# Kernel tuning notes

Hardware: AMD Instinct MI355X
Metric: run time of the kernel (lower is better)

The kernel has to match this reference:

```python
import jax, jax.numpy as jnp
import numpy as np

N_NODES = 100000
N_EDGES = 1600000
D_IN = 64
D_HID = 64
N_LAYERS = 3


def setup_inputs() -> dict:
    key = jax.random.key(0)
    ks = jax.random.split(key, 10)
    inp = {
        "node_feat": jax.random.normal(ks[0], (N_NODES, D_IN), dtype=jnp.float32),
        "src": jax.random.randint(ks[1], (N_EDGES,), 0, N_NODES, dtype=jnp.int32),
        "dst": jax.random.randint(ks[2], (N_EDGES,), 0, N_NODES, dtype=jnp.int32),
        "graph_len": jnp.ones((1,), dtype=jnp.int32) * N_NODES,
    }
    # GraphConv weights: shape (in_feats, out_feats), applied as feat @ W + b (DGL xavier-style init)
    dims = [D_IN] + [D_HID] * N_LAYERS
    for i in range(N_LAYERS):
        scale = float(np.sqrt(2.0 / (dims[i] + dims[i + 1])))
        inp[f"W{i}"] = jax.random.normal(ks[3 + i], (dims[i], dims[i + 1]), dtype=jnp.float32) * scale
        inp[f"b{i}"] = jnp.zeros((dims[i + 1],), dtype=jnp.float32)
    return inp


def reference(node_feat, src, dst, graph_len, W0, b0, W1, b1, W2, b2):
    n = node_feat.shape[0]
    e = src.shape[0]
    ones = jnp.ones((e,), dtype=node_feat.dtype)
    # DGL GraphConv norm='both': src-side out-degree^{-1/2}, dst-side in-degree^{-1/2}, clamp(min=1)
    deg_out = jax.ops.segment_sum(ones, src, num_segments=n)
    deg_in = jax.ops.segment_sum(ones, dst, num_segments=n)
    inv_sqrt_out = jax.lax.rsqrt(jnp.clip(deg_out, 1.0, None))[:, None]  # [N,1]
    inv_sqrt_in = jax.lax.rsqrt(jnp.clip(deg_in, 1.0, None))[:, None]    # [N,1]

    def graph_conv(x, W, b):
        msg = (x * inv_sqrt_out)[src]                              # [E,F] gather
        agg = jax.ops.segment_sum(msg, dst, num_segments=n)        # [N,F] scatter-add
        return (agg * inv_sqrt_in) @ W + b                         # SpMM result -> dense linear

    xs = []
    h = node_feat
    for W, b in ((W0, b0), (W1, b1), (W2, b2)):
        h = jax.nn.relu(graph_conv(h, W, b))
        xs.append(h)

    # Faithful to source: torch.sum(x, dim=1) -> per-node scalar [N]; concat over layers -> [3N]
    x_pool = jnp.concatenate([x.sum(axis=1) for x in xs], axis=-1)
    xs_cat = jnp.concatenate(xs, axis=-1)  # [N, 3*H]
    return x_pool, xs_cat
```

## Files before the change

kernel.cpp:

```cpp
#include <hip/hip_runtime.h>


#define TPB 256
#define CAPB 16384
#define CAP_S2 10240

__device__ __forceinline__ unsigned short f2bf(float f) {
  unsigned u = __float_as_uint(f);
  u += 0x7fff + ((u >> 16) & 1);
  return (unsigned short)(u >> 16);
}
__device__ __forceinline__ float bflo(unsigned u) { return __uint_as_float(u << 16); }
__device__ __forceinline__ float bfhi(unsigned u) { return __uint_as_float(u & 0xffff0000u); }

__global__ void init_cursors(int* __restrict__ cur_s, int* __restrict__ cur_d) {
  int t = threadIdx.x;
  cur_s[t] = t * CAPB;
  cur_d[t] = t * CAPB;
}

__global__ __launch_bounds__(256) void scatter_both(
    const int* __restrict__ src, const int* __restrict__ dst, int e,
    int* __restrict__ cur_s, int* __restrict__ cur_d,
    int* __restrict__ srcbuf, unsigned* __restrict__ edges1) {
  __shared__ int hs[256], hd[256];
  int t = threadIdx.x, b = blockIdx.x;
  hs[t] = 0; hd[t] = 0;
  __syncthreads();
  int base = b * 4096;
  int sv[16], dv[16];
  #pragma unroll
  for (int k = 0; k < 4; k++) {
    int i = base + 4 * t + 1024 * k;
    if (i + 3 < e) {
      int4 s4 = *(const int4*)&src[i];
      int4 d4 = *(const int4*)&dst[i];
      sv[4*k] = s4.x; sv[4*k+1] = s4.y; sv[4*k+2] = s4.z; sv[4*k+3] = s4.w;
      dv[4*k] = d4.x; dv[4*k+1] = d4.y; dv[4*k+2] = d4.z; dv[4*k+3] = d4.w;
    } else {
      #pragma unroll
      for (int j = 0; j < 4; j++) {
        int idx = i + j;
        if (idx < e) { sv[4*k+j] = src[idx]; dv[4*k+j] = dst[idx]; }
        else { sv[4*k+j] = -1; dv[4*k+j] = -1; }
      }
    }
  }
  #pragma unroll
  for (int k = 0; k < 16; k++) {
    if (dv[k] >= 0) {
      atomicAdd(&hs[sv[k] >> 9], 1);
      atomicAdd(&hd[dv[k] >> 9], 1);
    }
  }
  __syncthreads();
  int bs = hs[t], bd = hd[t];
  hs[t] = bs ? atomicAdd(&cur_s[t], bs) : 0;
  hd[t] = bd ? atomicAdd(&cur_d[t], bd) : 0;
  __syncthreads();
  #pragma unroll
  for (int k = 0; k < 16; k++) {
    if (dv[k] >= 0) {
      int ps = atomicAdd(&hs[sv[k] >> 9], 1);
      srcbuf[ps] = sv[k];
      int pd = atomicAdd(&hd[dv[k] >> 9], 1);
      edges1[pd] = ((unsigned)sv[k] << 9) | (unsigned)(dv[k] & 511);
    }
  }
}

__global__ __launch_bounds__(256) void sort_deg_cast(
    const unsigned* __restrict__ edges1, const int* __restrict__ srcbuf,
    const int* __restrict__ cur_s, const int* __restrict__ cur_d,
    const float* __restrict__ node_feat,
    int* __restrict__ row_beg, int* __restrict__ row_end,
    float* __restrict__ inv_in, float* __restrict__ inv_out,
    unsigned short* __restrict__ xb, int* __restrict__ col, int n) {
  __shared__ int sOut[CAP_S2];
  __shared__ int hist[512], cur[512];
  __shared__ int psum[256];
  __shared__ int dhist[512];
  __shared__ float sInv[512];
  int b = blockIdx.x, t = threadIdx.x;
  int sbase = b * CAPB;
  int es = cur_s[b];
  int ed = cur_d[b];
  int rstart = b << 9;
  int nrows = min(512, n - rstart);
  hist[t] = 0; hist[t + 256] = 0;
  dhist[t] = 0; dhist[t + 256] = 0;
  __syncthreads();
  for (int i = sbase + t; i < ed; i += TPB) atomicAdd(&hist[edges1[i] & 511u], 1);
  for (int i = sbase + t; i < es; i += TPB) atomicAdd(&dhist[srcbuf[i] & 511], 1);
  __syncthreads();
  #pragma unroll
  for (int k = 0; k < 2; k++) {
    int r = t + k * 256;
    if (r < nrows) {
      float iv = rsqrtf(fmaxf((float)dhist[r], 1.0f));
      sInv[r] = iv;
      inv_out[rstart + r] = iv;
    }
  }
  int h0 = hist[2 * t], h1 = hist[2 * t + 1];
  psum[t] = h0 + h1; __syncthreads();
  for (int off = 1; off < 256; off <<= 1) {
    int a = (t >= off) ? psum[t - off] : 0;
    __syncthreads(); psum[t] += a; __syncthreads();
  }
  int ex = psum[t] - (h0 + h1);
  cur[2 * t] = ex; cur[2 * t + 1] = ex + h0;
  if (2 * t < nrows) {
    row_beg[rstart + 2 * t] = sbase + ex;
    row_end[rstart + 2 * t] = sbase + ex + h0;
    inv_in[rstart + 2 * t] = rsqrtf(fmaxf((float)h0, 1.0f));
  }
  if (2 * t + 1 < nrows) {
    row_beg[rstart + 2 * t + 1] = sbase + ex + h0;
    row_end[rstart + 2 * t + 1] = sbase + ex + h0 + h1;
    inv_in[rstart + 2 * t + 1] = rsqrtf(fmaxf((float)h1, 1.0f));
  }
  __syncthreads();
  for (int i = sbase + t; i < ed; i += TPB) {
    unsigned v = edges1[i];
    int pos = atomicAdd(&cur[v & 511u], 1);
    int svv = (int)(v >> 9);
    if (pos < CAP_S2) sOut[pos] = svv;
    else col[sbase + pos] = svv;
  }
  __syncthreads();
  int m = min(ed - sbase, CAP_S2);
  for (int k = t; k < m; k += TPB) col[sbase + k] = sOut[k];
  int total4 = nrows * 16;
  const float* xbase = node_feat + (size_t)rstart * 64;
  unsigned short* obase = xb + (size_t)rstart * 64;
  for (int u = t; u < total4; u += TPB) {
    int r = u >> 4;
    float sc = sInv[r];
    float4 v = *(const float4*)&xbase[(size_t)u * 4];
    ushort4 o;
    o.x = f2bf(v.x * sc); o.y = f2bf(v.y * sc);
    o.z = f2bf(v.z * sc); o.w = f2bf(v.w * sc);
    *(ushort4*)&obase[(size_t)u * 4] = o;
  }
}

__global__ __launch_bounds__(256) void spmm_bf16(
    const unsigned short* __restrict__ xb,
    const int* __restrict__ row_beg, const int* __restrict__ row_end,
    const int* __restrict__ col,
    float* __restrict__ agg, int n) {
  int wid = (blockIdx.x * TPB + threadIdx.x) >> 6;
  if (wid >= n) return;
  int lane = threadIdx.x & 63;
  int g = lane >> 3;
  int l8 = (lane & 7) << 3;
  int s = row_beg[wid], e = row_end[wid];
  float a0 = 0, a1 = 0, a2 = 0, a3 = 0, a4 = 0, a5 = 0, a6 = 0, a7 = 0;
  for (int i = s + g; i < e; i += 32) {
    int ec = e - 1;
    int i1 = i + 8, i2 = i + 16, i3 = i + 24;
    int c0 = col[i];
    int c1 = col[min(i1, ec)];
    int c2 = col[min(i2, ec)];
    int c3 = col[min(i3, ec)];
    float m1 = (i1 < e) ? 1.f : 0.f;
    float m2 = (i2 < e) ? 1.f : 0.f;
    float m3 = (i3 < e) ? 1.f : 0.f;
    uint4 r0 = *(const uint4*)&xb[(size_t)c0 * 64 + l8];
    uint4 r1 = *(const uint4*)&xb[(size_t)c1 * 64 + l8];
    uint4 r2 = *(const uint4*)&xb[(size_t)c2 * 64 + l8];
    uint4 r3 = *(const uint4*)&xb[(size_t)c3 * 64 + l8];
    a0 += bflo(r0.x); a1 += bfhi(r0.x); a2 += bflo(r0.y); a3 += bfhi(r0.y);
    a4 += bflo(r0.z); a5 += bfhi(r0.z); a6 += bflo(r0.w); a7 += bfhi(r0.w);
    a0 = fmaf(m1, bflo(r1.x), a0); a1 = fmaf(m1, bfhi(r1.x), a1);
    a2 = fmaf(m1, bflo(r1.y), a2); a3 = fmaf(m1, bfhi(r1.y), a3);
    a4 = fmaf(m1, bflo(r1.z), a4); a5 = fmaf(m1, bfhi(r1.z), a5);
    a6 = fmaf(m1, bflo(r1.w), a6); a7 = fmaf(m1, bfhi(r1.w), a7);
    a0 = fmaf(m2, bflo(r2.x), a0); a1 = fmaf(m2, bfhi(r2.x), a1);
    a2 = fmaf(m2, bflo(r2.y), a2); a3 = fmaf(m2, bfhi(r2.y), a3);
    a4 = fmaf(m2, bflo(r2.z), a4); a5 = fmaf(m2, bfhi(r2.z), a5);
    a6 = fmaf(m2, bflo(r2.w), a6); a7 = fmaf(m2, bfhi(r2.w), a7);
    a0 = fmaf(m3, bflo(r3.x), a0); a1 = fmaf(m3, bfhi(r3.x), a1);
    a2 = fmaf(m3, bflo(r3.y), a2); a3 = fmaf(m3, bfhi(r3.y), a3);
    a4 = fmaf(m3, bflo(r3.z), a4); a5 = fmaf(m3, bfhi(r3.z), a5);
    a6 = fmaf(m3, bflo(r3.w), a6); a7 = fmaf(m3, bfhi(r3.w), a7);
  }
  a0 += __shfl_xor(a0, 8); a0 += __shfl_xor(a0, 16); a0 += __shfl_xor(a0, 32);
  a1 += __shfl_xor(a1, 8); a1 += __shfl_xor(a1, 16); a1 += __shfl_xor(a1, 32);
  a2 += __shfl_xor(a2, 8); a2 += __shfl_xor(a2, 16); a2 += __shfl_xor(a2, 32);
  a3 += __shfl_xor(a3, 8); a3 += __shfl_xor(a3, 16); a3 += __shfl_xor(a3, 32);
  a4 += __shfl_xor(a4, 8); a4 += __shfl_xor(a4, 16); a4 += __shfl_xor(a4, 32);
  a5 += __shfl_xor(a5, 8); a5 += __shfl_xor(a5, 16); a5 += __shfl_xor(a5, 32);
  a6 += __shfl_xor(a6, 8); a6 += __shfl_xor(a6, 16); a6 += __shfl_xor(a6, 32);
  a7 += __shfl_xor(a7, 8); a7 += __shfl_xor(a7, 16); a7 += __shfl_xor(a7, 32);
  if (g == 0) {
    float4 lo = {a0, a1, a2, a3};
    float4 hi = {a4, a5, a6, a7};
    *(float4*)&agg[(size_t)wid * 64 + l8] = lo;
    *(float4*)&agg[(size_t)wid * 64 + l8 + 4] = hi;
  }
}

__global__ __launch_bounds__(256) void gemm_relu_pool(
    const float* __restrict__ agg, const float* __restrict__ inv_in,
    const float* __restrict__ inv_out,
    const float* __restrict__ W, const float* __restrict__ bias,
    float* __restrict__ out_cat, float* __restrict__ out_pool,
    unsigned short* __restrict__ xb_next, int n) {
  __shared__ float sW[64 * 64];
  __shared__ float sXT[64][68];
  int t = threadIdx.x;
  int row0 = blockIdx.x * 64;
  for (int i4 = t * 4; i4 < 4096; i4 += 1024)
    *(float4*)&sW[i4] = *(const float4*)&W[i4];
  for (int i = t; i < 4096; i += TPB) {
    int r = i >> 6, f = i & 63;
    int row = row0 + r;
    sXT[f][r] = (row < n) ? agg[(size_t)row * 64 + f] * inv_in[row] : 0.f;
  }
  __syncthreads();
  int tj = t & 15, tr = t >> 4;
  int j4 = tj << 2, r4 = tr << 2;
  const float4 bv = *(const float4*)&bias[j4];
  float4 a0 = bv, a1 = bv, a2 = bv, a3 = bv;
  #pragma unroll 8
  for (int f = 0; f < 64; f++) {
    float4 w  = *(const float4*)&sW[f * 64 + j4];
    float4 xv = *(const float4*)&sXT[f][r4];
    a0.x = fmaf(xv.x, w.x, a0.x); a0.y = fmaf(xv.x, w.y, a0.y);
    a0.z = fmaf(xv.x, w.z, a0.z); a0.w = fmaf(xv.x, w.w, a0.w);
    a1.x = fmaf(xv.y, w.x, a1.x); a1.y = fmaf(xv.y, w.y, a1.y);
    a1.z = fmaf(xv.y, w.z, a1.z); a1.w = fmaf(xv.y, w.w, a1.w);
    a2.x = fmaf(xv.z, w.x, a2.x); a2.y = fmaf(xv.z, w.y, a2.y);
    a2.z = fmaf(xv.z, w.z, a2.z); a2.w = fmaf(xv.z, w.w, a2.w);
    a3.x = fmaf(xv.w, w.x, a3.x); a3.y = fmaf(xv.w, w.y, a3.y);
    a3.z = fmaf(xv.w, w.z, a3.z); a3.w = fmaf(xv.w, w.w, a3.w);
  }
  float4 accs[4] = {a0, a1, a2, a3};
  #pragma unroll
  for (int ri = 0; ri < 4; ri++) {
    int row = row0 + r4 + ri;
    if (row < n) {
      float4 h = accs[ri];
      h.x = fmaxf(h.x, 0.f); h.y = fmaxf(h.y, 0.f);
      h.z = fmaxf(h.z, 0.f); h.w = fmaxf(h.w, 0.f);
      *(float4*)&out_cat[(size_t)row * 192 + j4] = h;
      if (xb_next) {
        float sc = inv_out[row];
        ushort4 o;
        o.x = f2bf(h.x * sc); o.y = f2bf(h.y * sc);
        o.z = f2bf(h.z * sc); o.w = f2bf(h.w * sc);
        *(ushort4*)&xb_next[(size_t)row * 64 + j4] = o;
      }
      float part = h.x + h.y + h.z + h.w;
      part += __shfl_xor(part, 1);
      part += __shfl_xor(part, 2);
      part += __shfl_xor(part, 4);
      part += __shfl_xor(part, 8);
      if (tj == 0) out_pool[row] = part;
    }
  }
}


extern "C" void kernel_launch(void* const* d_in, const int* in_sizes, int n_in,
                              void* d_out, int out_size, void* d_ws, size_t ws_size,
                              hipStream_t stream) {
  const float* node_feat = (const float*)d_in[0];
  const int* src = (const int*)d_in[1];
  const int* dst = (const int*)d_in[2];
  const float* Ws[3] = {(const float*)d_in[4], (const float*)d_in[6], (const float*)d_in[8]};
  const float* bs[3] = {(const float*)d_in[5], (const float*)d_in[7], (const float*)d_in[9]};
  float* out = (float*)d_out;
  int n = in_sizes[0] / 64;
  int e = in_sizes[1];
  int nbb = (n + 511) >> 9;
  int nblk = (e + 4095) / 4096;
  size_t slots = (size_t)nbb * CAPB;

  char* p = (char*)d_ws;
  float* agg = (float*)p;       p += (size_t)n * 64 * sizeof(float);
  unsigned short* xb = (unsigned short*)p; p += (size_t)n * 64 * sizeof(unsigned short);
  float* inv_out = (float*)p;   p += (size_t)n * sizeof(float);
  float* inv_in = (float*)p;    p += (size_t)n * sizeof(float);
  int* row_beg = (int*)p;       p += (size_t)n * sizeof(int);
  int* row_end = (int*)p;       p += (size_t)n * sizeof(int);
  int* cur_s = (int*)p;         p += 256 * sizeof(int);
  int* cur_d = (int*)p;         p += 256 * sizeof(int);
  unsigned* edges1 = (unsigned*)p; p += slots * sizeof(unsigned);
  int* srcbuf = (int*)p;        p += slots * sizeof(int);
  int* col = (int*)p;           p += slots * sizeof(int);

  init_cursors<<<1, 256, 0, stream>>>(cur_s, cur_d);
  scatter_both<<<nblk, TPB, 0, stream>>>(src, dst, e, cur_s, cur_d, srcbuf, edges1);
  sort_deg_cast<<<nbb, TPB, 0, stream>>>(edges1, srcbuf, cur_s, cur_d, node_feat,
                                         row_beg, row_end, inv_in, inv_out, xb, col, n);

  float* cat_base = out + (size_t)3 * n;
  for (int layer = 0; layer < 3; layer++) {
    spmm_bf16<<<(n + 3) / 4, TPB, 0, stream>>>(xb, row_beg, row_end, col, agg, n);
    gemm_relu_pool<<<(n + 63) / 64, TPB, 0, stream>>>(agg, inv_in, inv_out, Ws[layer], bs[layer],
        cat_base + (size_t)layer * 64, out + (size_t)layer * n,
        (layer < 2) ? xb : (unsigned short*)nullptr, n);
  }
}
```

Baseline: 357.0 us.

## Fuse SpMM aggregation into the GEMM/ReLU/pool kernel with ping-pong bf16 buffers

The separate SpMM kernel and GEMM kernel are merged into one 512-thread kernel. Each wave aggregates 16 destination rows and writes the scaled sums straight into the shared-memory transposed tile, so the 128-row GEMM runs on it without the fp32 agg buffer ever going to global memory. Two bf16 feature buffers alternate between layers, because a layer now reads the previous features while it writes the next ones. This removes the agg global write and re-read and halves the number of launches. In exchange each wave processes its rows one after another before the block barrier, so fewer independent gathers are in flight and some latency hiding is lost.

```diff
diff --git a/kernel.cpp b/kernel.cpp
--- a/kernel.cpp
+++ b/kernel.cpp
@@ -145,79 +145,77 @@
   }
 }
 
-__global__ __launch_bounds__(256) void spmm_bf16(
+__global__ __launch_bounds__(512) void spmm_gemm(
     const unsigned short* __restrict__ xb,
     const int* __restrict__ row_beg, const int* __restrict__ row_end,
     const int* __restrict__ col,
-    float* __restrict__ agg, int n) {
-  int wid = (blockIdx.x * TPB + threadIdx.x) >> 6;
-  if (wid >= n) return;
-  int lane = threadIdx.x & 63;
-  int g = lane >> 3;
-  int l8 = (lane & 7) << 3;
-  int s = row_beg[wid], e = row_end[wid];
-  float a0 = 0, a1 = 0, a2 = 0, a3 = 0, a4 = 0, a5 = 0, a6 = 0, a7 = 0;
-  for (int i = s + g; i < e; i += 32) {
-    int ec = e - 1;
-    int i1 = i + 8, i2 = i + 16, i3 = i + 24;
-    int c0 = col[i];
-    int c1 = col[min(i1, ec)];
-    int c2 = col[min(i2, ec)];
-    int c3 = col[min(i3, ec)];
-    float m1 = (i1 < e) ? 1.f : 0.f;
-    float m2 = (i2 < e) ? 1.f : 0.f;
-    float m3 = (i3 < e) ? 1.f : 0.f;
-    uint4 r0 = *(const uint4*)&xb[(size_t)c0 * 64 + l8];
-    uint4 r1 = *(const uint4*)&xb[(size_t)c1 * 64 + l8];
-    uint4 r2 = *(const uint4*)&xb[(size_t)c2 * 64 + l8];
-    uint4 r3 = *(const uint4*)&xb[(size_t)c3 * 64 + l8];
-    a0 += bflo(r0.x); a1 += bfhi(r0.x); a2 += bflo(r0.y); a3 += bfhi(r0.y);
-    a4 += bflo(r0.z); a5 += bfhi(r0.z); a6 += bflo(r0.w); a7 += bfhi(r0.w);
-    a0 = fmaf(m1, bflo(r1.x), a0); a1 = fmaf(m1, bfhi(r1.x), a1);
-    a2 = fmaf(m1, bflo(r1.y), a2); a3 = fmaf(m1, bfhi(r1.y), a3);
-    a4 = fmaf(m1, bflo(r1.z), a4); a5 = fmaf(m1, bfhi(r1.z), a5);
-    a6 = fmaf(m1, bflo(r1.w), a6); a7 = fmaf(m1, bfhi(r1.w), a7);
-    a0 = fmaf(m2, bflo(r2.x), a0); a1 = fmaf(m2, bfhi(r2.x), a1);
-    a2 = fmaf(m2, bflo(r2.y), a2); a3 = fmaf(m2, bfhi(r2.y), a3);
-    a4 = fmaf(m2, bflo(r2.z), a4); a5 = fmaf(m2, bfhi(r2.z), a5);
-    a6 = fmaf(m2, bflo(r2.w), a6); a7 = fmaf(m2, bfhi(r2.w), a7);
-    a0 = fmaf(m3, bflo(r3.x), a0); a1 = fmaf(m3, bfhi(r3.x), a1);
-    a2 = fmaf(m3, bflo(r3.y), a2); a3 = fmaf(m3, bfhi(r3.y), a3);
-    a4 = fmaf(m3, bflo(r3.z), a4); a5 = fmaf(m3, bfhi(r3.z), a5);
-    a6 = fmaf(m3, bflo(r3.w), a6); a7 = fmaf(m3, bfhi(r3.w), a7);
-  }
-  a0 += __shfl_xor(a0, 8); a0 += __shfl_xor(a0, 16); a0 += __shfl_xor(a0, 32);
-  a1 += __shfl_xor(a1, 8); a1 += __shfl_xor(a1, 16); a1 += __shfl_xor(a1, 32);
-  a2 += __shfl_xor(a2, 8); a2 += __shfl_xor(a2, 16); a2 += __shfl_xor(a2, 32);
-  a3 += __shfl_xor(a3, 8); a3 += __shfl_xor(a3, 16); a3 += __shfl_xor(a3, 32);
-  a4 += __shfl_xor(a4, 8); a4 += __shfl_xor(a4, 16); a4 += __shfl_xor(a4, 32);
-  a5 += __shfl_xor(a5, 8); a5 += __shfl_xor(a5, 16); a5 += __shfl_xor(a5, 32);
-  a6 += __shfl_xor(a6, 8); a6 += __shfl_xor(a6, 16); a6 += __shfl_xor(a6, 32);
-  a7 += __shfl_xor(a7, 8); a7 += __shfl_xor(a7, 16); a7 += __shfl_xor(a7, 32);
-  if (g == 0) {
-    float4 lo = {a0, a1, a2, a3};
-    float4 hi = {a4, a5, a6, a7};
-    *(float4*)&agg[(size_t)wid * 64 + l8] = lo;
-    *(float4*)&agg[(size_t)wid * 64 + l8 + 4] = hi;
-  }
-}
-
-__global__ __launch_bounds__(256) void gemm_relu_pool(
-    const float* __restrict__ agg, const float* __restrict__ inv_in,
-    const float* __restrict__ inv_out,
+    const float* __restrict__ inv_in, const float* __restrict__ inv_out,
     const float* __restrict__ W, const float* __restrict__ bias,
     float* __restrict__ out_cat, float* __restrict__ out_pool,
     unsigned short* __restrict__ xb_next, int n) {
   __shared__ float sW[64 * 64];
-  __shared__ float sXT[64][68];
+  __shared__ float sXT[64][132];
   int t = threadIdx.x;
-  int row0 = blockIdx.x * 64;
-  for (int i4 = t * 4; i4 < 4096; i4 += 1024)
+  int row0 = blockIdx.x << 7;
+  for (int i4 = t * 4; i4 < 4096; i4 += 2048)
     *(float4*)&sW[i4] = *(const float4*)&W[i4];
-  for (int i = t; i < 4096; i += TPB) {
-    int r = i >> 6, f = i & 63;
-    int row = row0 + r;
-    sXT[f][r] = (row < n) ? agg[(size_t)row * 64 + f] * inv_in[row] : 0.f;
+  int lane = t & 63;
+  int g = lane >> 3;
+  int l8 = (lane & 7) << 3;
+  int wv = t >> 6;
+  for (int k = 0; k < 16; k++) {
+    int rl = wv * 16 + k;
+    int row = row0 + rl;
+    float v = 0.f;
+    if (row < n) {
+      float a0 = 0, a1 = 0, a2 = 0, a3 = 0, a4 = 0, a5 = 0, a6 = 0, a7 = 0;
+      int s = row_beg[row], e = row_end[row];
+      for (int i = s + g; i < e; i += 32) {
+        int ec = e - 1;
+        int i1 = i + 8, i2 = i + 16, i3 = i + 24;
+        int c0 = col[i];
+        int c1 = col[min(i1, ec)];
+        int c2 = col[min(i2, ec)];
+        int c3 = col[min(i3, ec)];
+        float m1 = (i1 < e) ? 1.f : 0.f;
+        float m2 = (i2 < e) ? 1.f : 0.f;
+        float m3 = (i3 < e) ? 1.f : 0.f;
+        uint4 r0 = *(const uint4*)&xb[(size_t)c0 * 64 + l8];
+        uint4 r1 = *(const uint4*)&xb[(size_t)c1 * 64 + l8];
+        uint4 r2 = *(const uint4*)&xb[(size_t)c2 * 64 + l8];
+        uint4 r3 = *(const uint4*)&xb[(size_t)c3 * 64 + l8];
+        a0 += bflo(r0.x); a1 += bfhi(r0.x); a2 += bflo(r0.y); a3 += bfhi(r0.y);
+        a4 += bflo(r0.z); a5 += bfhi(r0.z); a6 += bflo(r0.w); a7 += bfhi(r0.w);
+        a0 = fmaf(m1, bflo(r1.x), a0); a1 = fmaf(m1, bfhi(r1.x), a1);
+        a2 = fmaf(m1, bflo(r1.y), a2); a3 = fmaf(m1, bfhi(r1.y), a3);
+        a4 = fmaf(m1, bflo(r1.z), a4); a5 = fmaf(m1, bfhi(r1.z), a5);
+        a6 = fmaf(m1, bflo(r1.w), a6); a7 = fmaf(m1, bfhi(r1.w), a7);
+        a0 = fmaf(m2, bflo(r2.x), a0); a1 = fmaf(m2, bfhi(r2.x), a1);
+        a2 = fmaf(m2, bflo(r2.y), a2); a3 = fmaf(m2, bfhi(r2.y), a3);
+        a4 = fmaf(m2, bflo(r2.z), a4); a5 = fmaf(m2, bfhi(r2.z), a5);
+        a6 = fmaf(m2, bflo(r2.w), a6); a7 = fmaf(m2, bfhi(r2.w), a7);
+        a0 = fmaf(m3, bflo(r3.x), a0); a1 = fmaf(m3, bfhi(r3.x), a1);
+        a2 = fmaf(m3, bflo(r3.y), a2); a3 = fmaf(m3, bfhi(r3.y), a3);
+        a4 = fmaf(m3, bflo(r3.z), a4); a5 = fmaf(m3, bfhi(r3.z), a5);
+        a6 = fmaf(m3, bflo(r3.w), a6); a7 = fmaf(m3, bfhi(r3.w), a7);
+      }
+      a0 += __shfl_xor(a0, 8); a0 += __shfl_xor(a0, 16); a0 += __shfl_xor(a0, 32);
+      a1 += __shfl_xor(a1, 8); a1 += __shfl_xor(a1, 16); a1 += __shfl_xor(a1, 32);
+      a2 += __shfl_xor(a2, 8); a2 += __shfl_xor(a2, 16); a2 += __shfl_xor(a2, 32);
+      a3 += __shfl_xor(a3, 8); a3 += __shfl_xor(a3, 16); a3 += __shfl_xor(a3, 32);
+      a4 += __shfl_xor(a4, 8); a4 += __shfl_xor(a4, 16); a4 += __shfl_xor(a4, 32);
+      a5 += __shfl_xor(a5, 8); a5 += __shfl_xor(a5, 16); a5 += __shfl_xor(a5, 32);
+      a6 += __shfl_xor(a6, 8); a6 += __shfl_xor(a6, 16); a6 += __shfl_xor(a6, 32);
+      a7 += __shfl_xor(a7, 8); a7 += __shfl_xor(a7, 16); a7 += __shfl_xor(a7, 32);
+      float s0 = (g & 1) ? a1 : a0;
+      float s1 = (g & 1) ? a3 : a2;
+      float s2 = (g & 1) ? a5 : a4;
+      float s3 = (g & 1) ? a7 : a6;
+      float u0 = (g & 2) ? s1 : s0;
+      float u1 = (g & 2) ? s3 : s2;
+      v = ((g & 4) ? u1 : u0) * inv_in[row];
+    }
+    sXT[l8 + g][rl] = v;
   }
   __syncthreads();
   int tj = t & 15, tr = t >> 4;
@@ -280,8 +278,8 @@
   size_t slots = (size_t)nbb * CAPB;
 
   char* p = (char*)d_ws;
-  float* agg = (float*)p;       p += (size_t)n * 64 * sizeof(float);
-  unsigned short* xb = (unsigned short*)p; p += (size_t)n * 64 * sizeof(unsigned short);
+  unsigned short* xba = (unsigned short*)p; p += (size_t)n * 64 * sizeof(unsigned short);
+  unsigned short* xbb = (unsigned short*)p; p += (size_t)n * 64 * sizeof(unsigned short);
   float* inv_out = (float*)p;   p += (size_t)n * sizeof(float);
   float* inv_in = (float*)p;    p += (size_t)n * sizeof(float);
   int* row_beg = (int*)p;       p += (size_t)n * sizeof(int);
@@ -295,13 +293,14 @@
   init_cursors<<<1, 256, 0, stream>>>(cur_s, cur_d);
   scatter_both<<<nblk, TPB, 0, stream>>>(src, dst, e, cur_s, cur_d, srcbuf, edges1);
   sort_deg_cast<<<nbb, TPB, 0, stream>>>(edges1, srcbuf, cur_s, cur_d, node_feat,
-                                         row_beg, row_end, inv_in, inv_out, xb, col, n);
+                                         row_beg, row_end, inv_in, inv_out, xba, col, n);
 
   float* cat_base = out + (size_t)3 * n;
-  for (int layer = 0; layer < 3; layer++) {
-    spmm_bf16<<<(n + 3) / 4, TPB, 0, stream>>>(xb, row_beg, row_end, col, agg, n);
-    gemm_relu_pool<<<(n + 63) / 64, TPB, 0, stream>>>(agg, inv_in, inv_out, Ws[layer], bs[layer],
-        cat_base + (size_t)layer * 64, out + (size_t)layer * n,
-        (layer < 2) ? xb : (unsigned short*)nullptr, n);
-  }
-}
+  int nfb = (n + 127) >> 7;
+  spmm_gemm<<<nfb, 512, 0, stream>>>(xba, row_beg, row_end, col, inv_in, inv_out,
+      Ws[0], bs[0], cat_base + 0 * 64, out + (size_t)0 * n, xbb, n);
+  spmm_gemm<<<nfb, 512, 0, stream>>>(xbb, row_beg, row_end, col, inv_in, inv_out,
+      Ws[1], bs[1], cat_base + 1 * 64, out + (size_t)1 * n, xba, n);
+  spmm_gemm<<<nfb, 512, 0, stream>>>(xba, row_beg, row_end, col, inv_in, inv_out,
+      Ws[2], bs[2], cat_base + 2 * 64, out + (size_t)2 * n, (unsigned short*)nullptr, n);
+}
```

Result: slower. 382.8 us (+7.2%).
